# Optimization experiments

Hardware: AMD Instinct MI355X
Metric: run time of the kernel (lower is better)

## Reference

```python
import jax, jax.numpy as jnp
import numpy as np

N = 10000
E = 320000


def setup_inputs() -> dict:
    key = jax.random.key(0)
    ks = jax.random.split(key, 10)
    return {
        "x": jax.random.normal(ks[0], (N, 384), dtype=jnp.float32),
        "edge_index": jax.random.randint(ks[1], (2, E), 0, N, dtype=jnp.int64)
        if jax.config.jax_enable_x64 else jax.random.randint(ks[1], (2, E), 0, N, dtype=jnp.int32),
        "W1": jax.random.normal(ks[2], (256, 384), dtype=jnp.float32) * 0.05,
        "b1": jax.random.normal(ks[3], (256,), dtype=jnp.float32) * 0.05,
        "W2": jax.random.normal(ks[4], (128, 256), dtype=jnp.float32) * 0.05,
        "b2": jax.random.normal(ks[5], (128,), dtype=jnp.float32) * 0.05,
        "Wa1": jax.random.normal(ks[6], (64, 128), dtype=jnp.float32) * 0.05,
        "ba1": jax.random.normal(ks[7], (64,), dtype=jnp.float32) * 0.05,
        "Wa2": jax.random.normal(ks[8], (1, 64), dtype=jnp.float32) * 0.05,
        "ba2": jax.random.normal(ks[9], (1,), dtype=jnp.float32) * 0.05,
    }


def reference(x, edge_index, W1, b1, W2, b2, Wa1, ba1, Wa2, ba2):
    # fc1 + ReLU (dropout is identity in eval mode)
    h = jax.nn.relu(x @ W1.T + b1)  # (N, hidden)
    src, tgt = edge_index[0], edge_index[1]
    n = x.shape[0]
    # bincount(target, minlength=N) -> in-degree per node (constant across the 2 passes)
    deg = jax.ops.segment_sum(jnp.ones_like(tgt, dtype=h.dtype), tgt, num_segments=n)  # (N,)
    inv = 1.0 / (deg + 1.0)  # (N,)
    for _ in range(2):
        # gather neighbor features and scatter-add into target rows
        agg = jax.ops.segment_sum(h[src], tgt, num_segments=n)  # (N, hidden)
        h = 0.7 * h + 0.3 * agg * inv[:, None]
    out = jax.nn.relu(h @ W2.T + b2)  # (N, output_dim)
    # attention MLP: Linear -> ReLU -> Linear -> Sigmoid
    att = jax.nn.sigmoid(jax.nn.relu(out @ Wa1.T + ba1) @ Wa2.T + ba2)  # (N, 1)
    return out, att
```

## Files before the change

### kernel.cpp

```cpp
#include <hip/hip_runtime.h>
#include <hip/hip_bf16.h>
#include <math.h>

#define N_NODES 10000
#define E_EDGES 320000
#define F_IN    384
#define H1      256
#define H2      128
#define ATT1    64
#define DSTRIDE 128

typedef __attribute__((ext_vector_type(8))) short bf16x8;
typedef __attribute__((ext_vector_type(4))) float f32x4;

static __device__ inline unsigned short f2bf(float f) {
    unsigned u = __float_as_uint(f);
    unsigned r = (u + 0x7fffu + ((u >> 16) & 1u)) >> 16;
    return (unsigned short)r;
}

static __device__ inline unsigned pk2bf(float a, float b) {
    __hip_bfloat162 h2 = __float22bfloat162_rn(make_float2(a, b));
    return *reinterpret_cast<unsigned*>(&h2);
}

static __device__ inline float bflo(unsigned v) { return __uint_as_float(v << 16); }
static __device__ inline float bfhi(unsigned v) { return __uint_as_float(v & 0xffff0000u); }
static __device__ inline float bf2f(short s) {
    return __uint_as_float(((unsigned)(unsigned short)s) << 16);
}

__global__ void k_conv(const float* __restrict__ W1, const float* __restrict__ W2,
                       const float* __restrict__ Wa1,
                       unsigned short* __restrict__ w1b, unsigned short* __restrict__ w2b,
                       unsigned short* __restrict__ wa1b,
                       int* __restrict__ cursor) {
    const int n1 = H1 * F_IN / 4;
    const int n2 = H2 * H1 / 4;
    const int n3 = ATT1 * H2 / 4;
    const int nc = n1 + n2 + n3;
    int i = blockIdx.x * blockDim.x + threadIdx.x;
    if (i < nc) {
        const float4* src;
        ushort4* dst;
        int j;
        if (i < n1)           { src = (const float4*)W1;  dst = (ushort4*)w1b;  j = i; }
        else if (i < n1 + n2) { src = (const float4*)W2;  dst = (ushort4*)w2b;  j = i - n1; }
        else                  { src = (const float4*)Wa1; dst = (ushort4*)wa1b; j = i - n1 - n2; }
        float4 v = src[j];
        ushort4 o;
        o.x = f2bf(v.x); o.y = f2bf(v.y); o.z = f2bf(v.z); o.w = f2bf(v.w);
        dst[j] = o;
    } else {
        int j = i - nc;
        if (j < N_NODES / 4) ((int4*)cursor)[j] = make_int4(0, 0, 0, 0);
    }
}

#define NBLK_FC  (N_NODES / 16)
#define NBLK_FIL ((E_EDGES + 255) / 256)
#define S1 264
__global__ __launch_bounds__(256) void k_fc12fill(const float* __restrict__ x,
                                                  const unsigned short* __restrict__ w1b,
                                                  const float* __restrict__ b1,
                                                  const unsigned short* __restrict__ w2b,
                                                  unsigned short* __restrict__ z,
                                                  const int* __restrict__ srcv,
                                                  const int* __restrict__ tgt,
                                                  int* __restrict__ cursor,
                                                  int* __restrict__ csrf) {
    __shared__ unsigned short sh[16 * S1];
    if (blockIdx.x >= NBLK_FC) {
        int e = (blockIdx.x - NBLK_FC) * 256 + threadIdx.x;
        if (e < E_EDGES) {
            int t = tgt[e];
            int p = atomicAdd(&cursor[t], 1);
            if (p < DSTRIDE) csrf[t * DSTRIDE + p] = srcv[e];
        }
        return;
    }
    int wave = threadIdx.x >> 6;
    int lane = threadIdx.x & 63;
    int m0 = blockIdx.x * 16;
    int ml = lane & 15, quad = lane >> 4;
    {
        int nbase = wave * 64;
        const float* Ar = x + (size_t)(m0 + ml) * F_IN + quad * 8;
        const bf16x8* Brow[4];
        #pragma unroll
        for (int j = 0; j < 4; j++)
            Brow[j] = (const bf16x8*)(w1b + (size_t)(nbase + j * 16 + ml) * F_IN + quad * 8);
        f32x4 acc[4] = {{0,0,0,0},{0,0,0,0},{0,0,0,0},{0,0,0,0}};
        for (int kk = 0; kk < F_IN / 32; kk++) {
            float4 f0 = *(const float4*)(Ar + kk * 32);
            float4 f1 = *(const float4*)(Ar + kk * 32 + 4);
            bf16x8 a;
            ((unsigned*)&a)[0] = pk2bf(f0.x, f0.y);
            ((unsigned*)&a)[1] = pk2bf(f0.z, f0.w);
            ((unsigned*)&a)[2] = pk2bf(f1.x, f1.y);
            ((unsigned*)&a)[3] = pk2bf(f1.z, f1.w);
            #pragma unroll
            for (int j = 0; j < 4; j++) {
                bf16x8 b = Brow[j][kk * 4];
                acc[j] = __builtin_amdgcn_mfma_f32_16x16x32_bf16(a, b, acc[j], 0, 0, 0);
            }
        }
        #pragma unroll
        for (int j = 0; j < 4; j++) {
            int col = nbase + j * 16 + ml;
            float bb = b1[col];
            #pragma unroll
            for (int r = 0; r < 4; r++) {
                int lr = quad * 4 + r;
                float v = acc[j][r] + bb;
                sh[lr * S1 + col] = f2bf(v > 0.f ? v : 0.f);
            }
        }
    }
    __syncthreads();
    {
        int c0 = wave * 32;
        const unsigned short* pA = sh + ml * S1 + quad * 8;
        const bf16x8* B0 = (const bf16x8*)(w2b + (size_t)(c0 + ml) * H1 + quad * 8);
        const bf16x8* B1 = (const bf16x8*)(w2b + (size_t)(c0 + 16 + ml) * H1 + quad * 8);
        f32x4 za0 = {0,0,0,0}, za1 = {0,0,0,0};
        #pragma unroll
        for (int kk = 0; kk < H1 / 32; kk++) {
            bf16x8 a = *(const bf16x8*)(pA + kk * 32);
            bf16x8 b0 = B0[kk * 4];
            bf16x8 b1 = B1[kk * 4];
            za0 = __builtin_amdgcn_mfma_f32_16x16x32_bf16(a, b0, za0, 0, 0, 0);
            za1 = __builtin_amdgcn_mfma_f32_16x16x32_bf16(a, b1, za1, 0, 0, 0);
        }
        #pragma unroll
        for (int r = 0; r < 4; r++) {
            int row = m0 + quad * 4 + r;
            z[(size_t)row * H2 + c0 + ml] = f2bf(za0[r]);
            z[(size_t)row * H2 + c0 + 16 + ml] = f2bf(za1[r]);
        }
    }
}

__global__ __launch_bounds__(256) void k_agg1(const unsigned short* __restrict__ zin,
                                              unsigned short* __restrict__ zout,
                                              const int* __restrict__ cursor,
                                              const int* __restrict__ csrf) {
    int t = blockIdx.x * 4 + (threadIdx.x >> 6);
    int tid = threadIdx.x & 63;
    int dg = cursor[t];
    if (dg > DSTRIDE) dg = DSTRIDE;
    const unsigned* base = (const unsigned*)zin;
    float a0 = 0.f, a1 = 0.f, b0 = 0.f, b1 = 0.f;
    for (int e0 = 0; e0 < dg; e0 += 64) {
        int cnt = dg - e0; if (cnt > 64) cnt = 64;
        int c = (e0 + tid < dg) ? csrf[t * DSTRIDE + e0 + tid] : 0;
        int j = 0;
        for (; j + 8 <= cnt; j += 8) {
            unsigned v0 = base[(size_t)__builtin_amdgcn_readlane(c, j    ) * 64 + tid];
            unsigned v1 = base[(size_t)__builtin_amdgcn_readlane(c, j + 1) * 64 + tid];
            unsigned v2 = base[(size_t)__builtin_amdgcn_readlane(c, j + 2) * 64 + tid];
            unsigned v3 = base[(size_t)__builtin_amdgcn_readlane(c, j + 3) * 64 + tid];
            unsigned v4 = base[(size_t)__builtin_amdgcn_readlane(c, j + 4) * 64 + tid];
            unsigned v5 = base[(size_t)__builtin_amdgcn_readlane(c, j + 5) * 64 + tid];
            unsigned v6 = base[(size_t)__builtin_amdgcn_readlane(c, j + 6) * 64 + tid];
            unsigned v7 = base[(size_t)__builtin_amdgcn_readlane(c, j + 7) * 64 + tid];
            a0 += bflo(v0); a1 += bfhi(v0);  b0 += bflo(v1); b1 += bfhi(v1);
            a0 += bflo(v2); a1 += bfhi(v2);  b0 += bflo(v3); b1 += bfhi(v3);
            a0 += bflo(v4); a1 += bfhi(v4);  b0 += bflo(v5); b1 += bfhi(v5);
            a0 += bflo(v6); a1 += bfhi(v6);  b0 += bflo(v7); b1 += bfhi(v7);
        }
        for (; j < cnt; j++) {
            unsigned v = base[(size_t)__builtin_amdgcn_readlane(c, j) * 64 + tid];
            a0 += bflo(v); a1 += bfhi(v);
        }
    }
    a0 += b0; a1 += b1;
    unsigned sv = base[(size_t)t * 64 + tid];
    float iv = 0.3f / (float)(dg + 1);
    float r0 = 0.7f * bflo(sv) + iv * a0;
    float r1 = 0.7f * bfhi(sv) + iv * a1;
    ((unsigned*)zout)[(size_t)t * 64 + tid] = pk2bf(r0, r1);
}

__global__ __launch_bounds__(256) void k_agg2fin(const unsigned short* __restrict__ zin,
                                                 const int* __restrict__ cursor,
                                                 const int* __restrict__ csrf,
                                                 const float* __restrict__ b2,
                                                 const unsigned short* __restrict__ wa1b,
                                                 const float* __restrict__ ba1,
                                                 const float* __restrict__ Wa2,
                                                 const float* __restrict__ ba2,
                                                 float* __restrict__ out,
                                                 float* __restrict__ att) {
    __shared__ float sout[4][128];
    int nl = threadIdx.x >> 6;
    int t = blockIdx.x * 4 + nl;
    int tid = threadIdx.x & 63;
    int dg = cursor[t];
    if (dg > DSTRIDE) dg = DSTRIDE;
    const unsigned* base = (const unsigned*)zin;
    float a0 = 0.f, a1 = 0.f, b0a = 0.f, b1a = 0.f;
    for (int e0 = 0; e0 < dg; e0 += 64) {
        int cnt = dg - e0; if (cnt > 64) cnt = 64;
        int c = (e0 + tid < dg) ? csrf[t * DSTRIDE + e0 + tid] : 0;
        int j = 0;
        for (; j + 8 <= cnt; j += 8) {
            unsigned v0 = base[(size_t)__builtin_amdgcn_readlane(c, j    ) * 64 + tid];
            unsigned v1 = base[(size_t)__builtin_amdgcn_readlane(c, j + 1) * 64 + tid];
            unsigned v2 = base[(size_t)__builtin_amdgcn_readlane(c, j + 2) * 64 + tid];
            unsigned v3 = base[(size_t)__builtin_amdgcn_readlane(c, j + 3) * 64 + tid];
            unsigned v4 = base[(size_t)__builtin_amdgcn_readlane(c, j + 4) * 64 + tid];
            unsigned v5 = base[(size_t)__builtin_amdgcn_readlane(c, j + 5) * 64 + tid];
            unsigned v6 = base[(size_t)__builtin_amdgcn_readlane(c, j + 6) * 64 + tid];
            unsigned v7 = base[(size_t)__builtin_amdgcn_readlane(c, j + 7) * 64 + tid];
            a0 += bflo(v0); a1 += bfhi(v0);  b0a += bflo(v1); b1a += bfhi(v1);
            a0 += bflo(v2); a1 += bfhi(v2);  b0a += bflo(v3); b1a += bfhi(v3);
            a0 += bflo(v4); a1 += bfhi(v4);  b0a += bflo(v5); b1a += bfhi(v5);
            a0 += bflo(v6); a1 += bfhi(v6);  b0a += bflo(v7); b1a += bfhi(v7);
        }
        for (; j < cnt; j++) {
            unsigned v = base[(size_t)__builtin_amdgcn_readlane(c, j) * 64 + tid];
            a0 += bflo(v); a1 += bfhi(v);
        }
    }
    a0 += b0a; a1 += b1a;
    unsigned sv = base[(size_t)t * 64 + tid];
    float iv = 0.3f / (float)(dg + 1);
    float2 bb = *(const float2*)(b2 + 2 * tid);
    float f0 = 0.7f * bflo(sv) + iv * a0 + bb.x;  f0 = f0 > 0.f ? f0 : 0.f;
    float f1 = 0.7f * bfhi(sv) + iv * a1 + bb.y;  f1 = f1 > 0.f ? f1 : 0.f;
    *(float2*)(out + (size_t)t * H2 + 2 * tid) = make_float2(f0, f1);
    *(float2*)(&sout[nl][2 * tid]) = make_float2(f0, f1);
    float acc = ba1[tid];
    const bf16x8* wrow = (const bf16x8*)(wa1b + (size_t)tid * H2);
    const float* srow = sout[nl];
    #pragma unroll
    for (int k8 = 0; k8 < 16; k8++) {
        bf16x8 w = wrow[k8];
        #pragma unroll
        for (int u = 0; u < 8; u++)
            acc += bf2f(w[u]) * srow[k8 * 8 + u];
    }
    float g = (acc > 0.f ? acc : 0.f) * Wa2[tid];
    #pragma unroll
    for (int d = 1; d < 64; d <<= 1) g += __shfl_xor(g, d, 64);
    if (tid == 0) att[t] = 1.f / (1.f + expf(-g));
}

extern "C" void kernel_launch(void* const* d_in, const int* in_sizes, int n_in,
                              void* d_out, int out_size, void* d_ws, size_t ws_size,
                              hipStream_t stream) {
    const float* x   = (const float*)d_in[0];
    const int*   ei  = (const int*)d_in[1];
    const float* W1  = (const float*)d_in[2];
    const float* b1  = (const float*)d_in[3];
    const float* W2  = (const float*)d_in[4];
    const float* b2  = (const float*)d_in[5];
    const float* Wa1 = (const float*)d_in[6];
    const float* ba1 = (const float*)d_in[7];
    const float* Wa2 = (const float*)d_in[8];
    const float* ba2 = (const float*)d_in[9];
    const int* srcv = ei;
    const int* tgt  = ei + E_EDGES;

    float* out_mat = (float*)d_out;
    float* att     = out_mat + N_NODES * H2;

    unsigned short* w1b  = (unsigned short*)d_ws;
    unsigned short* w2b  = w1b + (size_t)H1 * F_IN;
    unsigned short* wa1b = w2b + (size_t)H2 * H1;
    unsigned short* z0   = wa1b + (size_t)ATT1 * H2;
    unsigned short* z1   = z0 + (size_t)N_NODES * H2;
    int* cursor = (int*)(z1 + (size_t)N_NODES * H2);
    int* csrf   = cursor + N_NODES;

    {
        const int nc = (H1 * F_IN + H2 * H1 + ATT1 * H2) / 4;
        int total = nc + N_NODES / 4;
        k_conv<<<(total + 255) / 256, 256, 0, stream>>>(W1, W2, Wa1, w1b, w2b, wa1b, cursor);
    }

    k_fc12fill<<<NBLK_FC + NBLK_FIL, 256, 0, stream>>>(x, w1b, b1, w2b, z0,
                                                       srcv, tgt, cursor, csrf);

    k_agg1<<<N_NODES / 4, 256, 0, stream>>>(z0, z1, cursor, csrf);

    k_agg2fin<<<N_NODES / 4, 256, 0, stream>>>(z1, cursor, csrf, b2,
                                               wa1b, ba1, Wa2, ba2, out_mat, att);
}
```

Before: 157.7 us.

## Pre-swizzle weights into MFMA fragment order and stage x tile in LDS

The weight conversion kernel now writes W1 and W2 in bf16, laid out in MFMA fragment order, so each lane reads a contiguous 16-byte chunk per k-step rather than strided row slices. The fc1 stage loads and converts the 16x384 x tile into shared memory once with coalesced float4 loads, instead of each wave converting its own strided global reads. The edge-fill blocks each handle 1024 edges with nontemporal stores to the CSR buffer. In exchange, the shared footprint grows and the kernel gains an extra barrier.

```diff
diff --git a/kernel.cpp b/kernel.cpp
--- a/kernel.cpp
+++ b/kernel.cpp
@@ -30,35 +30,55 @@
     return __uint_as_float(((unsigned)(unsigned short)s) << 16);
 }
 
+#define NW1 (H1 * F_IN / 8)
+#define NW2 (H2 * H1 / 8)
+#define NWA (ATT1 * H2 / 4)
+#define NCZ (N_NODES / 4)
 __global__ void k_conv(const float* __restrict__ W1, const float* __restrict__ W2,
                        const float* __restrict__ Wa1,
                        unsigned short* __restrict__ w1b, unsigned short* __restrict__ w2b,
                        unsigned short* __restrict__ wa1b,
                        int* __restrict__ cursor) {
-    const int n1 = H1 * F_IN / 4;
-    const int n2 = H2 * H1 / 4;
-    const int n3 = ATT1 * H2 / 4;
-    const int nc = n1 + n2 + n3;
     int i = blockIdx.x * blockDim.x + threadIdx.x;
-    if (i < nc) {
-        const float4* src;
-        ushort4* dst;
-        int j;
-        if (i < n1)           { src = (const float4*)W1;  dst = (ushort4*)w1b;  j = i; }
-        else if (i < n1 + n2) { src = (const float4*)W2;  dst = (ushort4*)w2b;  j = i - n1; }
-        else                  { src = (const float4*)Wa1; dst = (ushort4*)wa1b; j = i - n1 - n2; }
-        float4 v = src[j];
+    if (i < NW1) {
+        int s = i;
+        int jb = s / 768, rem = s - jb * 768;
+        int kk = rem >> 6, lane = rem & 63;
+        int ml = lane & 15, quad = lane >> 4;
+        const float* p = W1 + (size_t)(jb * 16 + ml) * F_IN + kk * 32 + quad * 8;
+        float4 u0 = *(const float4*)p;
+        float4 u1 = *(const float4*)(p + 4);
+        uint4 o;
+        o.x = pk2bf(u0.x, u0.y); o.y = pk2bf(u0.z, u0.w);
+        o.z = pk2bf(u1.x, u1.y); o.w = pk2bf(u1.z, u1.w);
+        ((uint4*)w1b)[s] = o;
+    } else if (i < NW1 + NW2) {
+        int s = i - NW1;
+        int jcol = s / 512, rem = s - jcol * 512;
+        int kk = rem >> 6, lane = rem & 63;
+        int ml = lane & 15, quad = lane >> 4;
+        const float* p = W2 + (size_t)(jcol * 16 + ml) * H1 + kk * 32 + quad * 8;
+        float4 u0 = *(const float4*)p;
+        float4 u1 = *(const float4*)(p + 4);
+        uint4 o;
+        o.x = pk2bf(u0.x, u0.y); o.y = pk2bf(u0.z, u0.w);
+        o.z = pk2bf(u1.x, u1.y); o.w = pk2bf(u1.z, u1.w);
+        ((uint4*)w2b)[s] = o;
+    } else if (i < NW1 + NW2 + NWA) {
+        int j = i - NW1 - NW2;
+        float4 v = ((const float4*)Wa1)[j];
         ushort4 o;
         o.x = f2bf(v.x); o.y = f2bf(v.y); o.z = f2bf(v.z); o.w = f2bf(v.w);
-        dst[j] = o;
+        ((ushort4*)wa1b)[j] = o;
     } else {
-        int j = i - nc;
-        if (j < N_NODES / 4) ((int4*)cursor)[j] = make_int4(0, 0, 0, 0);
+        int j = i - NW1 - NW2 - NWA;
+        if (j < NCZ) ((int4*)cursor)[j] = make_int4(0, 0, 0, 0);
     }
 }
 
 #define NBLK_FC  (N_NODES / 16)
-#define NBLK_FIL ((E_EDGES + 255) / 256)
+#define NBLK_FIL ((E_EDGES + 1023) / 1024)
+#define XS 392
 #define S1 264
 __global__ __launch_bounds__(256) void k_fc12fill(const float* __restrict__ x,
                                                   const unsigned short* __restrict__ w1b,
@@ -69,13 +89,18 @@
                                                   const int* __restrict__ tgt,
                                                   int* __restrict__ cursor,
                                                   int* __restrict__ csrf) {
-    __shared__ unsigned short sh[16 * S1];
+    __shared__ unsigned short smem[16 * XS];
     if (blockIdx.x >= NBLK_FC) {
-        int e = (blockIdx.x - NBLK_FC) * 256 + threadIdx.x;
-        if (e < E_EDGES) {
-            int t = tgt[e];
-            int p = atomicAdd(&cursor[t], 1);
-            if (p < DSTRIDE) csrf[t * DSTRIDE + p] = srcv[e];
+        int e0 = (blockIdx.x - NBLK_FC) * 1024 + threadIdx.x;
+        #pragma unroll
+        for (int q = 0; q < 4; q++) {
+            int e = e0 + q * 256;
+            if (e < E_EDGES) {
+                int t = tgt[e];
+                int p = atomicAdd(&cursor[t], 1);
+                if (p < DSTRIDE)
+                    __builtin_nontemporal_store(srcv[e], &csrf[t * DSTRIDE + p]);
+            }
         }
         return;
     }
@@ -84,51 +109,55 @@
     int m0 = blockIdx.x * 16;
     int ml = lane & 15, quad = lane >> 4;
     {
-        int nbase = wave * 64;
-        const float* Ar = x + (size_t)(m0 + ml) * F_IN + quad * 8;
-        const bf16x8* Brow[4];
-        #pragma unroll
-        for (int j = 0; j < 4; j++)
-            Brow[j] = (const bf16x8*)(w1b + (size_t)(nbase + j * 16 + ml) * F_IN + quad * 8);
-        f32x4 acc[4] = {{0,0,0,0},{0,0,0,0},{0,0,0,0},{0,0,0,0}};
+        const float4* xsrc = (const float4*)(x + (size_t)m0 * F_IN);
+        #pragma unroll
+        for (int r = 0; r < 6; r++) {
+            int idx = r * 256 + threadIdx.x;
+            float4 v = xsrc[idx];
+            int row = idx / 96, c4 = idx - row * 96;
+            unsigned* sp = (unsigned*)(smem + row * XS + c4 * 4);
+            sp[0] = pk2bf(v.x, v.y);
+            sp[1] = pk2bf(v.z, v.w);
+        }
+    }
+    __syncthreads();
+    f32x4 acc[4] = {{0,0,0,0},{0,0,0,0},{0,0,0,0},{0,0,0,0}};
+    {
+        const unsigned short* ax = smem + ml * XS + quad * 8;
+        const bf16x8* W1f = (const bf16x8*)w1b;
         for (int kk = 0; kk < F_IN / 32; kk++) {
-            float4 f0 = *(const float4*)(Ar + kk * 32);
-            float4 f1 = *(const float4*)(Ar + kk * 32 + 4);
-            bf16x8 a;
-            ((unsigned*)&a)[0] = pk2bf(f0.x, f0.y);
-            ((unsigned*)&a)[1] = pk2bf(f0.z, f0.w);
-            ((unsigned*)&a)[2] = pk2bf(f1.x, f1.y);
-            ((unsigned*)&a)[3] = pk2bf(f1.z, f1.w);
+            bf16x8 a = *(const bf16x8*)(ax + kk * 32);
             #pragma unroll
             for (int j = 0; j < 4; j++) {
-                bf16x8 b = Brow[j][kk * 4];
+                int jb = wave * 4 + j;
+                bf16x8 b = W1f[(jb * 12 + kk) * 64 + lane];
                 acc[j] = __builtin_amdgcn_mfma_f32_16x16x32_bf16(a, b, acc[j], 0, 0, 0);
             }
         }
-        #pragma unroll
-        for (int j = 0; j < 4; j++) {
-            int col = nbase + j * 16 + ml;
-            float bb = b1[col];
-            #pragma unroll
-            for (int r = 0; r < 4; r++) {
-                int lr = quad * 4 + r;
-                float v = acc[j][r] + bb;
-                sh[lr * S1 + col] = f2bf(v > 0.f ? v : 0.f);
-            }
+    }
+    __syncthreads();
+    #pragma unroll
+    for (int j = 0; j < 4; j++) {
+        int col = wave * 64 + j * 16 + ml;
+        float bb = b1[col];
+        #pragma unroll
+        for (int r = 0; r < 4; r++) {
+            int lr = quad * 4 + r;
+            float v = acc[j][r] + bb;
+            smem[lr * S1 + col] = f2bf(v > 0.f ? v : 0.f);
         }
     }
     __syncthreads();
     {
         int c0 = wave * 32;
-        const unsigned short* pA = sh + ml * S1 + quad * 8;
-        const bf16x8* B0 = (const bf16x8*)(w2b + (size_t)(c0 + ml) * H1 + quad * 8);
-        const bf16x8* B1 = (const bf16x8*)(w2b + (size_t)(c0 + 16 + ml) * H1 + quad * 8);
+        const unsigned short* pA = smem + ml * S1 + quad * 8;
+        const bf16x8* W2f = (const bf16x8*)w2b;
         f32x4 za0 = {0,0,0,0}, za1 = {0,0,0,0};
         #pragma unroll
         for (int kk = 0; kk < H1 / 32; kk++) {
             bf16x8 a = *(const bf16x8*)(pA + kk * 32);
-            bf16x8 b0 = B0[kk * 4];
-            bf16x8 b1 = B1[kk * 4];
+            bf16x8 b0 = W2f[((wave * 2 + 0) * 8 + kk) * 64 + lane];
+            bf16x8 b1 = W2f[((wave * 2 + 1) * 8 + kk) * 64 + lane];
             za0 = __builtin_amdgcn_mfma_f32_16x16x32_bf16(a, b0, za0, 0, 0, 0);
             za1 = __builtin_amdgcn_mfma_f32_16x16x32_bf16(a, b1, za1, 0, 0, 0);
         }
@@ -275,8 +304,7 @@
     int* csrf   = cursor + N_NODES;
 
     {
-        const int nc = (H1 * F_IN + H2 * H1 + ATT1 * H2) / 4;
-        int total = nc + N_NODES / 4;
+        int total = NW1 + NW2 + NWA + NCZ;
         k_conv<<<(total + 255) / 256, 256, 0, stream>>>(W1, W2, Wa1, w1b, w2b, wa1b, cursor);
     }
 
```

Result: faster. 145.1 us (-8.0%).
